# Performance work log

Measured on AMD Instinct MI355X. Metric: run time of the kernel, lower is better.

## Reference

```python
import jax, jax.numpy as jnp
import numpy as np

N, C, H, W = 8, 3, 720, 1280


def setup_inputs() -> dict:
    key = jax.random.key(0)
    k1, k2 = jax.random.split(key)
    image = jax.random.normal(k1, (N, C, H, W), dtype=jnp.float32)
    # scale flow so integer truncation gives real displacements (and collisions)
    flow = jax.random.normal(k2, (N, 2, H, W), dtype=jnp.float32) * 20.0
    return {"image": image, "flow": flow}


def _warp_fw(image, flow):
    n, c, h, w = image.shape
    hw = h * w
    # flat source mesh coordinates (same for all batches)
    mx = jnp.broadcast_to(jnp.arange(w, dtype=jnp.int32)[None, :], (h, w)).reshape(-1)
    my = jnp.broadcast_to(jnp.arange(h, dtype=jnp.int32)[:, None], (h, w)).reshape(-1)
    fx = flow[:, 0].reshape(n, hw)
    fy = flow[:, 1].reshape(n, hw)
    # torch .long() truncates toward zero; astype(int32) matches
    wx = jnp.clip(mx[None, :] + fx.astype(jnp.int32), 0, w - 1)
    wy = jnp.clip(my[None, :] + fy.astype(jnp.int32), 0, h - 1)
    tgt = wy * w + wx  # (n, hw) linear target index
    v = fx * fx + fy * fy
    sortidx = jnp.argsort(v, axis=1)  # (n, hw) ascending
    ranks = jnp.arange(hw, dtype=jnp.int32)

    def per_batch(sortidx_i, tgt_i):
        # rank[p] = position of source pixel p in the sorted write order
        rank = jnp.zeros((hw,), jnp.int32).at[sortidx_i].set(ranks)
        # winning (max) rank at each target location; -1 = hole
        best = jnp.full((hw,), -1, jnp.int32).at[tgt_i].max(rank)
        covered = best >= 0
        # winning source pixel index = sortidx[best_rank]
        src = jnp.take(sortidx_i, jnp.clip(best, 0, hw - 1))
        return src, covered

    src, covered = jax.vmap(per_batch)(sortidx, tgt)  # (n, hw) each
    img_flat = image.reshape(n, c, hw)
    gathered = jnp.take_along_axis(
        img_flat, jnp.broadcast_to(src[:, None, :], (n, c, hw)), axis=2
    )
    out = jnp.where(covered[:, None, :], gathered, 0.0)
    return out.reshape(n, c, h, w)


def reference(image, flow):
    return _warp_fw(image, flow)
```

## Files before the change

### kernel.cpp

```cpp
#include <hip/hip_runtime.h>
#include <cstdint>

constexpr int N_ = 8;
constexpr int C_ = 3;
constexpr int H_ = 720;
constexpr int W_ = 1280;
constexpr int HW = H_ * W_;

constexpr int TW = 128;
constexpr int TH = 64;
constexpr int M_ = 96;
constexpr int NTX = W_ / TW;
constexpr int NTY = (H_ + TH - 1) / TH;
constexpr int BLK = 512;
constexpr int OCAP = 4096;

typedef float vf4 __attribute__((ext_vector_type(4)));

struct Outlier { unsigned long long key; int n; int tgt; };

__device__ __forceinline__ unsigned long long make_key(float fx, float fy, int p) {
    float v = __fadd_rn(__fmul_rn(fx, fx), __fmul_rn(fy, fy));
    return ((unsigned long long)__float_as_uint(v) << 32) | (unsigned int)(p + 1);
}

__global__ __launch_bounds__(256) void outlier_kernel(
    const float* __restrict__ flow,
    unsigned long long* __restrict__ ocnt,
    Outlier* __restrict__ olist) {
    int idx = blockIdx.x * 256 + threadIdx.x;
    int n = idx / (HW / 4);
    int p0 = (idx - n * (HW / 4)) * 4;
    const float* f = flow + (size_t)n * 2 * HW;
    vf4 fx4 = *(const vf4*)(f + p0);
    vf4 fy4 = *(const vf4*)(f + HW + p0);
    float fxs[4] = {fx4.x, fx4.y, fx4.z, fx4.w};
    float fys[4] = {fy4.x, fy4.y, fy4.z, fy4.w};
    int y = p0 / W_;
    int x0 = p0 - y * W_;
    #pragma unroll
    for (int i = 0; i < 4; ++i) {
        int dx = (int)fxs[i];
        int dy = (int)fys[i];
        if (dx > M_ || dx < -M_ || dy > M_ || dy < -M_) {
            int wx = min(max(x0 + i + dx, 0), W_ - 1);
            int wy = min(max(y + dy, 0), H_ - 1);
            unsigned long long o = atomicAdd(ocnt, 1ULL);
            if (o < (unsigned long long)OCAP) {
                Outlier e;
                e.key = make_key(fxs[i], fys[i], p0 + i);
                e.n = n;
                e.tgt = wy * W_ + wx;
                olist[o] = e;
            }
        }
    }
}

__global__ __launch_bounds__(BLK, 4) void warp_tile_kernel(
    const float* __restrict__ image,
    const float* __restrict__ flow,
    const unsigned long long* __restrict__ ocnt,
    const Outlier* __restrict__ olist,
    float* __restrict__ out) {
    __shared__ unsigned long long lkey[TH * TW];
    int tx0 = blockIdx.x * TW;
    int ty0 = blockIdx.y * TH;
    int n   = blockIdx.z;
    int th_eff = min(TH, H_ - ty0);
    int tid = threadIdx.x;

    for (int i = tid; i < TH * TW; i += BLK) lkey[i] = 0ULL;
    __syncthreads();

    int wy0 = max(0, ty0 - M_), wy1 = min(H_, ty0 + th_eff + M_);
    int wx0 = max(0, tx0 - M_), wx1 = min(W_, tx0 + TW + M_);
    int gx = (wx1 - wx0) >> 2;
    int total = gx * (wy1 - wy0);
    const float* fx_p = flow + (size_t)n * 2 * HW;
    const float* fy_p = fx_p + HW;

    for (int g = tid; g < total; g += BLK) {
        int gy = g / gx;
        int gxx = g - gy * gx;
        int y = wy0 + gy;
        int x4 = wx0 + 4 * gxx;
        int pbase = y * W_ + x4;
        vf4 fx4 = *(const vf4*)(fx_p + pbase);
        vf4 fy4 = *(const vf4*)(fy_p + pbase);
        float fxs[4] = {fx4.x, fx4.y, fx4.z, fx4.w};
        float fys[4] = {fy4.x, fy4.y, fy4.z, fy4.w};
        #pragma unroll
        for (int i = 0; i < 4; ++i) {
            float fx = fxs[i], fy = fys[i];
            int wx = x4 + i + (int)fx;
            int wy = y + (int)fy;
            wx = min(max(wx, 0), W_ - 1);
            wy = min(max(wy, 0), H_ - 1);
            int lx = wx - tx0, ly = wy - ty0;
            if ((unsigned)lx < (unsigned)TW && (unsigned)ly < (unsigned)th_eff) {
                atomicMax(&lkey[ly * TW + lx], make_key(fx, fy, pbase + i));
            }
        }
    }
    __syncthreads();

    unsigned long long craw = *ocnt;
    int cnt = (int)(craw > (unsigned long long)OCAP ? OCAP : craw);
    for (int o = tid; o < cnt; o += BLK) {
        Outlier e = olist[o];
        if (e.n == n) {
            int ey = e.tgt / W_, ex = e.tgt - (e.tgt / W_) * W_;
            int lx = ex - tx0, ly = ey - ty0;
            if ((unsigned)lx < (unsigned)TW && (unsigned)ly < (unsigned)th_eff)
                atomicMax(&lkey[ly * TW + lx], e.key);
        }
    }
    __syncthreads();

    const float* img_n = image + (size_t)n * C_ * HW;
    float* out_n = out + (size_t)n * C_ * HW;
    int q4 = th_eff * (TW / 4);
    for (int s = tid; s < q4; s += BLK) {
        int r = s >> 5;
        int cg = s & 31;
        int lp = r * TW + cg * 4;
        unsigned long long k0 = lkey[lp],     k1 = lkey[lp + 1];
        unsigned long long k2 = lkey[lp + 2], k3 = lkey[lp + 3];
        int s0 = (int)(unsigned int)(k0 & 0xffffffffULL) - 1;
        int s1 = (int)(unsigned int)(k1 & 0xffffffffULL) - 1;
        int s2 = (int)(unsigned int)(k2 & 0xffffffffULL) - 1;
        int s3 = (int)(unsigned int)(k3 & 0xffffffffULL) - 1;
        int op = (ty0 + r) * W_ + tx0 + cg * 4;
        #pragma unroll
        for (int c = 0; c < C_; ++c) {
            const float* pl = img_n + (size_t)c * HW;
            vf4 o;
            o.x = k0 ? pl[s0] : 0.0f;
            o.y = k1 ? pl[s1] : 0.0f;
            o.z = k2 ? pl[s2] : 0.0f;
            o.w = k3 ? pl[s3] : 0.0f;
            __builtin_nontemporal_store(o, (vf4*)(out_n + (size_t)c * HW + op));
        }
    }
}

extern "C" void kernel_launch(void* const* d_in, const int* in_sizes, int n_in,
                              void* d_out, int out_size, void* d_ws, size_t ws_size,
                              hipStream_t stream) {
    const float* image = (const float*)d_in[0];
    const float* flow  = (const float*)d_in[1];
    float* out = (float*)d_out;

    unsigned long long* ocnt = (unsigned long long*)d_ws;
    Outlier* olist = (Outlier*)((char*)d_ws + 64);

    (void)hipMemsetAsync(ocnt, 0, sizeof(unsigned long long), stream);

    int k0_blocks = (N_ * HW / 4) / 256;
    outlier_kernel<<<k0_blocks, 256, 0, stream>>>(flow, ocnt, olist);

    dim3 grid(NTX, NTY, N_);
    warp_tile_kernel<<<grid, BLK, 0, stream>>>(image, flow, ocnt, olist, out);
}
```

Before: 337.0 us.

## Shrink halo margin, double block size, restructure scatter loop to fixed 2D thread mapping

Reduces the halo margin from 96 to 64 so each tile scans fewer flow pixels, and routes more source pixels to the global outlier list, whose capacity grows to 65536. The block grows to 1024 threads with a fixed mapping of 64 column groups by 16 row stripes, replacing per-iteration division with a simple stride loop. Shared memory clear and key reads are vectorised to 128-bit accesses. Risks: columns whose x4 falls outside the image are skipped and rows beyond a multiple of 16 are dropped, which may lose writes at the borders, and with sigma-20 flow the outlier list may overflow.

```diff
diff --git a/kernel.cpp b/kernel.cpp
--- a/kernel.cpp
+++ b/kernel.cpp
@@ -9,13 +9,15 @@
 
 constexpr int TW = 128;
 constexpr int TH = 64;
-constexpr int M_ = 96;
+constexpr int M_ = 64;
 constexpr int NTX = W_ / TW;
 constexpr int NTY = (H_ + TH - 1) / TH;
-constexpr int BLK = 512;
-constexpr int OCAP = 4096;
+constexpr int BLK = 1024;
+constexpr int GX  = (TW + 2 * M_) / 4;
+constexpr int OCAP = 65536;
 
 typedef float vf4 __attribute__((ext_vector_type(4)));
+typedef unsigned long long vu2 __attribute__((ext_vector_type(2)));
 
 struct Outlier { unsigned long long key; int n; int tgt; };
 
@@ -57,7 +59,7 @@
     }
 }
 
-__global__ __launch_bounds__(BLK, 4) void warp_tile_kernel(
+__global__ __launch_bounds__(BLK, 8) void warp_tile_kernel(
     const float* __restrict__ image,
     const float* __restrict__ flow,
     const unsigned long long* __restrict__ ocnt,
@@ -70,36 +72,40 @@
     int th_eff = min(TH, H_ - ty0);
     int tid = threadIdx.x;
 
-    for (int i = tid; i < TH * TW; i += BLK) lkey[i] = 0ULL;
+    {
+        vu2 z = {0ULL, 0ULL};
+        #pragma unroll
+        for (int i = 0; i < 4; ++i) *((vu2*)lkey + tid + i * BLK) = z;
+    }
     __syncthreads();
 
-    int wy0 = max(0, ty0 - M_), wy1 = min(H_, ty0 + th_eff + M_);
-    int wx0 = max(0, tx0 - M_), wx1 = min(W_, tx0 + TW + M_);
-    int gx = (wx1 - wx0) >> 2;
-    int total = gx * (wy1 - wy0);
+    int gxx = tid & (GX - 1);
+    int gy0 = tid >> 6;
+    int x4 = tx0 - M_ + 4 * gxx;
+    int wy0 = max(0, ty0 - M_);
+    int wy1 = min(H_, ty0 + th_eff + M_);
+    int kmax = (wy1 - wy0) >> 4;
     const float* fx_p = flow + (size_t)n * 2 * HW;
     const float* fy_p = fx_p + HW;
 
-    for (int g = tid; g < total; g += BLK) {
-        int gy = g / gx;
-        int gxx = g - gy * gx;
-        int y = wy0 + gy;
-        int x4 = wx0 + 4 * gxx;
-        int pbase = y * W_ + x4;
-        vf4 fx4 = *(const vf4*)(fx_p + pbase);
-        vf4 fy4 = *(const vf4*)(fy_p + pbase);
-        float fxs[4] = {fx4.x, fx4.y, fx4.z, fx4.w};
-        float fys[4] = {fy4.x, fy4.y, fy4.z, fy4.w};
-        #pragma unroll
-        for (int i = 0; i < 4; ++i) {
-            float fx = fxs[i], fy = fys[i];
-            int wx = x4 + i + (int)fx;
-            int wy = y + (int)fy;
-            wx = min(max(wx, 0), W_ - 1);
-            wy = min(max(wy, 0), H_ - 1);
-            int lx = wx - tx0, ly = wy - ty0;
-            if ((unsigned)lx < (unsigned)TW && (unsigned)ly < (unsigned)th_eff) {
-                atomicMax(&lkey[ly * TW + lx], make_key(fx, fy, pbase + i));
+    if ((unsigned)x4 <= (unsigned)(W_ - 4)) {
+        for (int k = 0; k < kmax; ++k) {
+            int y = wy0 + gy0 + (k << 4);
+            int pbase = y * W_ + x4;
+            vf4 fx4 = *(const vf4*)(fx_p + pbase);
+            vf4 fy4 = *(const vf4*)(fy_p + pbase);
+            float fxs[4] = {fx4.x, fx4.y, fx4.z, fx4.w};
+            float fys[4] = {fy4.x, fy4.y, fy4.z, fy4.w};
+            #pragma unroll
+            for (int i = 0; i < 4; ++i) {
+                float fx = fxs[i], fy = fys[i];
+                int wx = x4 + i + (int)fx;
+                int wy = y + (int)fy;
+                wx = min(max(wx, 0), W_ - 1);
+                wy = min(max(wy, 0), H_ - 1);
+                int lx = wx - tx0, ly = wy - ty0;
+                if ((unsigned)lx < (unsigned)TW && (unsigned)ly < (unsigned)th_eff)
+                    atomicMax(&lkey[ly * TW + lx], make_key(fx, fy, pbase + i));
             }
         }
     }
@@ -125,8 +131,9 @@
         int r = s >> 5;
         int cg = s & 31;
         int lp = r * TW + cg * 4;
-        unsigned long long k0 = lkey[lp],     k1 = lkey[lp + 1];
-        unsigned long long k2 = lkey[lp + 2], k3 = lkey[lp + 3];
+        vu2 k01 = *(const vu2*)&lkey[lp];
+        vu2 k23 = *(const vu2*)&lkey[lp + 2];
+        unsigned long long k0 = k01.x, k1 = k01.y, k2 = k23.x, k3 = k23.y;
         int s0 = (int)(unsigned int)(k0 & 0xffffffffULL) - 1;
         int s1 = (int)(unsigned int)(k1 & 0xffffffffULL) - 1;
         int s2 = (int)(unsigned int)(k2 & 0xffffffffULL) - 1;
```

Measured after the change: 495.4 us. +47.0%, slower.
